# Performance work log

Measured on AMD Instinct MI355X. Metric: run time of the kernel, lower is better.

## Reference

```python
import jax, jax.numpy as jnp
import numpy as np

N, D_IN, D_OUT = 10000, 256, 256


def setup_inputs() -> dict:
    key = jax.random.key(0)
    k1, k2, k3, k4 = jax.random.split(key, 4)
    # xavier_uniform with gain=1.414 (as in the torch module)
    def xavier(k, shape, gain=1.414):
        fan_in, fan_out = shape[0], shape[1]
        bound = gain * np.sqrt(6.0 / (fan_in + fan_out))
        return jax.random.uniform(k, shape, jnp.float32, -bound, bound)
    return {
        "input": jax.random.normal(k1, (N, D_IN), jnp.float32),
        "adj": jax.random.randint(k2, (N, N), 0, 2, jnp.int32),  # binary dense adjacency
        "M": N,
        "W": xavier(k3, (D_IN, D_OUT)),
        "b": jnp.zeros((D_OUT,), jnp.float32),
        "a": xavier(k4, (D_OUT, 1)),
    }


def reference(input, adj, M, W, b, a):
    # h = tanh(X W + b); values used for attention logits
    h = jnp.tanh(input @ W + b)          # [N, F]
    inp = input @ W                      # [N, F] (values to aggregate)
    e = (h @ a)[:, 0]                    # [N] per-node logit
    # original also drops neighbors whose h row sums to exactly 0
    valid = (jnp.sum(h, axis=1) != 0)    # [N]
    mask = (adj[:M] > 0) & valid[None, :]  # [M, N]
    neg = jnp.asarray(-1e30, h.dtype)
    scores = jnp.where(mask, e[None, :], neg)           # [M, N]
    m = jnp.max(scores, axis=1, keepdims=True)
    w = jnp.where(mask, jnp.exp(scores - m), 0.0)       # masked exp
    denom = jnp.sum(w, axis=1, keepdims=True)
    att = w / jnp.maximum(denom, 1e-30)  # rows with no neighbors -> all zeros (matches torch zeros init)
    # dropout is identity in eval mode (training=False)
    return att @ inp                     # [M, F]
```

## Files before the change

### kernel.cpp

```cpp
#include <hip/hip_runtime.h>
#include <hip/hip_bf16.h>
#include <cstdint>
#include <cstddef>

#define NN      10000
#define DD      256
#define KSTEPS  313
#define MB2     79
#define KSPLIT  6

typedef __bf16 bf16x8 __attribute__((ext_vector_type(8)));
typedef float  f32x4  __attribute__((ext_vector_type(4)));

#define XG_OFF   0ull
#define XG_SIZE  (32ull * 10000 * 16)
#define WG_OFF   (XG_OFF + XG_SIZE)
#define WG_SIZE  (32ull * 256 * 16)
#define INP_OFF  (WG_OFF + WG_SIZE)
#define INP_SIZE (10000ull * 256 * 4)
#define E_OFF    (INP_OFF + INP_SIZE)
#define E_SIZE   (10016ull * 4)
#define HS_OFF   (E_OFF + E_SIZE)
#define HS_SIZE  (10016ull * 4)
#define G_OFF    (HS_OFF + HS_SIZE)
#define G_SIZE   (10016ull * 4)
#define YG_OFF   (G_OFF + G_SIZE + 256ull)
#define YG_SIZE  (318ull * 1088 * 16)
#define PN_OFF   (YG_OFF + YG_SIZE)
#define PN_SIZE  ((size_t)KSPLIT * 10000 * 272 * 4)

__device__ __forceinline__ void gl_lds16(const void* g, void* lds) {
    __builtin_amdgcn_global_load_lds(
        (const __attribute__((address_space(1))) unsigned int*)g,
        (__attribute__((address_space(3))) unsigned int*)lds,
        16, 0, 0);
}

__global__ __launch_bounds__(256) void k_build_xg(const float* __restrict__ X,
                                                  bf16x8* __restrict__ XG) {
    int idx = blockIdx.x * 256 + threadIdx.x;
    int row = idx >> 5;
    int q   = idx & 31;
    const float* src = X + row * 256 + q * 8;
    bf16x8 v;
#pragma unroll
    for (int j = 0; j < 8; ++j) v[j] = (__bf16)src[j];
    XG[q * 10000 + row] = v;
}

__global__ __launch_bounds__(256) void k_build_wg(const float* __restrict__ W,
                                                  bf16x8* __restrict__ WG) {
    int e = blockIdx.x * 256 + threadIdx.x;
    int q = e >> 8;
    int n = e & 255;
    bf16x8 v;
#pragma unroll
    for (int j = 0; j < 8; ++j) v[j] = (__bf16)W[(q * 8 + j) * 256 + n];
    WG[e] = v;
}

__global__ __launch_bounds__(256) void k_gemm1(const bf16x8* __restrict__ XG,
                                               const bf16x8* __restrict__ WG,
                                               const float* __restrict__ bvec,
                                               const float* __restrict__ avec,
                                               float* __restrict__ inp,
                                               float* __restrict__ evec,
                                               float* __restrict__ hsumv) {
    __shared__ bf16x8 Ash[320];
    __shared__ bf16x8 Bsh[1024];
    __shared__ float ePart[4][80];
    __shared__ float hPart[4][80];
    int tid = threadIdx.x, wid = tid >> 6, lane = tid & 63;
    int l15 = lane & 15, l4 = lane >> 4;
    int mb = blockIdx.x;

    f32x4 acc[4][5];
#pragma unroll
    for (int c = 0; c < 4; ++c)
#pragma unroll
        for (int rt = 0; rt < 5; ++rt) acc[c][rt] = f32x4{0.f, 0.f, 0.f, 0.f};

    for (int kb = 0; kb < 8; ++kb) {
        for (int rr = wid; rr < 5; rr += 4) {
            int c = rr * 64 + lane;
            int g = c / 80, r = c - g * 80;
            gl_lds16(XG + ((kb * 4 + g) * 10000 + mb * 80 + r), (char*)Ash + rr * 1024);
        }
        for (int rr = wid; rr < 16; rr += 4)
            gl_lds16(WG + kb * 1024 + rr * 64 + lane, (char*)Bsh + rr * 1024);
        __syncthreads();

        bf16x8 af[5];
#pragma unroll
        for (int rt = 0; rt < 5; ++rt) af[rt] = Ash[l4 * 80 + rt * 16 + l15];
#pragma unroll
        for (int c = 0; c < 4; ++c) {
            bf16x8 bf = Bsh[l4 * 256 + (wid * 4 + c) * 16 + l15];
#pragma unroll
            for (int rt = 0; rt < 5; ++rt)
                acc[c][rt] = __builtin_amdgcn_mfma_f32_16x16x32_bf16(af[rt], bf, acc[c][rt], 0, 0, 0);
        }
        __syncthreads();
    }

    float pe[5][4], ph[5][4];
#pragma unroll
    for (int rt = 0; rt < 5; ++rt)
#pragma unroll
        for (int rg = 0; rg < 4; ++rg) { pe[rt][rg] = 0.f; ph[rt][rg] = 0.f; }

#pragma unroll
    for (int c = 0; c < 4; ++c) {
        int col = (wid * 4 + c) * 16 + l15;
        float av = avec[col];
        float bv = bvec[col];
#pragma unroll
        for (int rt = 0; rt < 5; ++rt) {
#pragma unroll
            for (int rg = 0; rg < 4; ++rg) {
                int row = mb * 80 + rt * 16 + l4 * 4 + rg;
                float v = acc[c][rt][rg];
                inp[row * 256 + col] = v;
                float h = tanhf(v + bv);
                pe[rt][rg] += h * av;
                ph[rt][rg] += h;
            }
        }
    }
#pragma unroll
    for (int rt = 0; rt < 5; ++rt) {
#pragma unroll
        for (int rg = 0; rg < 4; ++rg) {
            float se = pe[rt][rg], sh = ph[rt][rg];
#pragma unroll
            for (int m = 1; m < 16; m <<= 1) {
                se += __shfl_xor(se, m);
                sh += __shfl_xor(sh, m);
            }
            if (l15 == 0) {
                int lr = rt * 16 + l4 * 4 + rg;
                ePart[wid][lr] = se;
                hPart[wid][lr] = sh;
            }
        }
    }
    __syncthreads();
    if (tid < 80) {
        float e = ePart[0][tid] + ePart[1][tid] + ePart[2][tid] + ePart[3][tid];
        float h = hPart[0][tid] + hPart[1][tid] + hPart[2][tid] + hPart[3][tid];
        evec[mb * 80 + tid] = e;
        hsumv[mb * 80 + tid] = h;
    }
}

__global__ __launch_bounds__(1024) void k_softmax_g(const float* __restrict__ evec,
                                                    const float* __restrict__ hsumv,
                                                    float* __restrict__ gv) {
    __shared__ float red[1024];
    int tid = threadIdx.x;
    float m = -3.0e38f;
    for (int i = tid; i < NN; i += 1024)
        if (hsumv[i] != 0.0f) m = fmaxf(m, evec[i]);
    red[tid] = m;
    __syncthreads();
    for (int s = 512; s > 0; s >>= 1) {
        if (tid < s) red[tid] = fmaxf(red[tid], red[tid + s]);
        __syncthreads();
    }
    float gmax = red[0];
    if (gmax < -1.0e37f) gmax = 0.0f;
    for (int i = tid; i < 10016; i += 1024) {
        float g = 0.0f;
        if (i < NN && hsumv[i] != 0.0f) g = expf(evec[i] - gmax);
        gv[i] = g;
    }
}

__global__ __launch_bounds__(256) void k_build_yg(const float* __restrict__ inp,
                                                  const float* __restrict__ gv,
                                                  bf16x8* __restrict__ YG) {
    int kb = blockIdx.x;
    for (int c = threadIdx.x; c < 1088; c += 256) {
        int gq = c / 272, n = c - gq * 272;
        int k0 = kb * 32 + gq * 8;
        bf16x8 v;
#pragma unroll
        for (int j = 0; j < 8; ++j) {
            int k = k0 + j;
            float val = 0.0f;
            if (k < NN) {
                float gk = gv[k];
                if (n < 256) val = gk * inp[k * 256 + n];
                else if (n == 256) val = gk;
            }
            v[j] = (__bf16)val;
        }
        YG[kb * 1088 + c] = v;
    }
}

__device__ __forceinline__ bf16x8 cvt_adj(int4 a, int4 b) {
    union { bf16x8 v; unsigned int u[4]; } r;
    r.u[0] = (a.x > 0 ? 0x3F80u : 0u) | (a.y > 0 ? 0x3F800000u : 0u);
    r.u[1] = (a.z > 0 ? 0x3F80u : 0u) | (a.w > 0 ? 0x3F800000u : 0u);
    r.u[2] = (b.x > 0 ? 0x3F80u : 0u) | (b.y > 0 ? 0x3F800000u : 0u);
    r.u[3] = (b.z > 0 ? 0x3F80u : 0u) | (b.w > 0 ? 0x3F800000u : 0u);
    return r.v;
}

__global__ __launch_bounds__(256, 2) void k_attn_gemm(const int* __restrict__ adj,
                                                      const bf16x8* __restrict__ YG,
                                                      float* __restrict__ pnum) {
    __shared__ int    Ash[2][4096];
    __shared__ bf16x8 Bsh[2][1088];
    int tid = threadIdx.x, wid = tid >> 6, lane = tid & 63;
    int l15 = lane & 15, l4 = lane >> 4;

    int orig = blockIdx.x;
    const int nwg = MB2 * KSPLIT, q = nwg >> 3, r = nwg & 7;
    int x = orig & 7, o = orig >> 3;
    int logical = (x < r ? x * (q + 1) : r * (q + 1) + (x - r) * q) + o;
    int kc = logical / MB2, mb = logical % MB2;
    int s0 = (kc * KSTEPS) / KSPLIT, s1 = ((kc + 1) * KSTEPS) / KSPLIT;

    const int* aSrc[4];
    int aLim[4];
#pragma unroll
    for (int i = 0; i < 4; ++i) {
        int c = (wid + i * 4) * 64 + lane;
        int row = c >> 3;
        int p = c & 7;
        int ck4 = (p ^ (row & 7)) * 4;
        int grow = min(mb * 128 + row, NN - 1);
        aSrc[i] = adj + (size_t)grow * 10000 + ck4;
        aLim[i] = 9996 - ck4;
    }

    f32x4 acc[2][17];
#pragma unroll
    for (int t = 0; t < 2; ++t)
#pragma unroll
        for (int ct = 0; ct < 17; ++ct) acc[t][ct] = f32x4{0.f, 0.f, 0.f, 0.f};

    auto stageA = [&](int sTile, int bufIdx) {
        int kk = sTile * 32;
        char* dst = (char*)&Ash[bufIdx][0];
#pragma unroll
        for (int i = 0; i < 4; ++i)
            gl_lds16(aSrc[i] + min(kk, aLim[i]), dst + (wid + i * 4) * 1024);
    };
    auto stageB = [&](int sTile, int bufIdx) {
        const bf16x8* src = YG + (size_t)sTile * 1088;
        char* dst = (char*)&Bsh[bufIdx][0];
#pragma unroll
        for (int i = 0; i < 5; ++i) {
            int rr = wid + i * 4;
            if (rr < 17) gl_lds16(src + rr * 64 + lane, dst + rr * 1024);
        }
    };

    int xr = l15 & 7;
    int p0 = (2 * l4) ^ xr;
    int rowA0 = wid * 32 + l15;

    stageA(s0, 0);
    stageB(s0, 0);
    __syncthreads();

    int buf = 0;
    for (int s = s0; s < s1; ++s) {
        if (s + 1 < s1) {
            stageA(s + 1, buf ^ 1);
            stageB(s + 1, buf ^ 1);
        }
        const int* ab = &Ash[buf][0];
        int4 v00 = *(const int4*)(ab + rowA0 * 32 + p0 * 4);
        int4 v01 = *(const int4*)(ab + rowA0 * 32 + (p0 ^ 1) * 4);
        int4 v10 = *(const int4*)(ab + (rowA0 + 16) * 32 + p0 * 4);
        int4 v11 = *(const int4*)(ab + (rowA0 + 16) * 32 + (p0 ^ 1) * 4);
        bf16x8 fa0 = cvt_adj(v00, v01);
        bf16x8 fa1 = cvt_adj(v10, v11);
#pragma unroll
        for (int ct = 0; ct < 17; ++ct) {
            bf16x8 fb = Bsh[buf][l4 * 272 + ct * 16 + l15];
            acc[0][ct] = __builtin_amdgcn_mfma_f32_16x16x32_bf16(fa0, fb, acc[0][ct], 0, 0, 0);
            acc[1][ct] = __builtin_amdgcn_mfma_f32_16x16x32_bf16(fa1, fb, acc[1][ct], 0, 0, 0);
        }
        __syncthreads();
        buf ^= 1;
    }

    float* base = pnum + (size_t)kc * 10000 * 272;
    int r0 = mb * 128 + wid * 32;
#pragma unroll
    for (int t = 0; t < 2; ++t) {
#pragma unroll
        for (int ct = 0; ct < 17; ++ct) {
            int col = ct * 16 + l15;
#pragma unroll
            for (int rg = 0; rg < 4; ++rg) {
                int row = r0 + t * 16 + l4 * 4 + rg;
                if (row < NN) base[(size_t)row * 272 + col] = acc[t][ct][rg];
            }
        }
    }
}

__global__ __launch_bounds__(256) void k_finalize(const float* __restrict__ pnum,
                                                  float* __restrict__ out) {
    int idx = blockIdx.x * 256 + threadIdx.x;
    int i = idx >> 6, q = idx & 63;
    float4 sv = {0.f, 0.f, 0.f, 0.f};
    float den = 0.f;
#pragma unroll
    for (int kc = 0; kc < KSPLIT; ++kc) {
        const float* row = pnum + ((size_t)kc * 10000 + i) * 272;
        float4 v = ((const float4*)row)[q];
        sv.x += v.x; sv.y += v.y; sv.z += v.z; sv.w += v.w;
        den += row[256];
    }
    float r = 1.0f / fmaxf(den, 1e-30f);
    float4 o;
    o.x = sv.x * r; o.y = sv.y * r; o.z = sv.z * r; o.w = sv.w * r;
    ((float4*)(out + (size_t)i * 256))[q] = o;
}

extern "C" void kernel_launch(void* const* d_in, const int* in_sizes, int n_in,
                              void* d_out, int out_size, void* d_ws, size_t ws_size,
                              hipStream_t stream) {
    const float* X    = (const float*)d_in[0];
    const int*   adj  = (const int*)d_in[1];
    const float* W    = (const float*)d_in[3];
    const float* bvec = (const float*)d_in[4];
    const float* avec = (const float*)d_in[5];
    float* out = (float*)d_out;

    char* ws = (char*)d_ws;
    bf16x8* XG   = (bf16x8*)(ws + XG_OFF);
    bf16x8* WG   = (bf16x8*)(ws + WG_OFF);
    float*  inp  = (float*)(ws + INP_OFF);
    float*  evec = (float*)(ws + E_OFF);
    float*  hsv  = (float*)(ws + HS_OFF);
    float*  gv   = (float*)(ws + G_OFF);
    bf16x8* YG   = (bf16x8*)(ws + YG_OFF);
    float*  pnum = (float*)(ws + PN_OFF);

    k_build_xg<<<1250, 256, 0, stream>>>(X, XG);
    k_build_wg<<<32, 256, 0, stream>>>(W, WG);
    k_gemm1<<<125, 256, 0, stream>>>(XG, WG, bvec, avec, inp, evec, hsv);
    k_softmax_g<<<1, 1024, 0, stream>>>(evec, hsv, gv);
    k_build_yg<<<318, 256, 0, stream>>>(inp, gv, YG);
    k_attn_gemm<<<MB2 * KSPLIT, 256, 0, stream>>>(adj, YG, pnum);
    k_finalize<<<2500, 256, 0, stream>>>(pnum, out);
}
```

Baseline: 191.8 us.

## Fuse prep kernels and replace single-block softmax with atomic global max

Merges the X and W bf16 repacking kernels into one launch, which also zeroes a global max slot. The per-block max of valid logits is now computed inside gemm1 and combined with an order-preserving atomicMax. The exp weights are computed on the fly inside build_yg. This removes two launches, including a serial single-block reduction, at the cost of an atomic per gemm1 block and redundant per-block exp work.

```diff
diff --git a/kernel.cpp b/kernel.cpp
--- a/kernel.cpp
+++ b/kernel.cpp
@@ -22,9 +22,9 @@
 #define E_SIZE   (10016ull * 4)
 #define HS_OFF   (E_OFF + E_SIZE)
 #define HS_SIZE  (10016ull * 4)
-#define G_OFF    (HS_OFF + HS_SIZE)
-#define G_SIZE   (10016ull * 4)
-#define YG_OFF   (G_OFF + G_SIZE + 256ull)
+#define GM_OFF   (HS_OFF + HS_SIZE)
+#define GM_SIZE  (256ull)
+#define YG_OFF   (GM_OFF + GM_SIZE)
 #define YG_SIZE  (318ull * 1088 * 16)
 #define PN_OFF   (YG_OFF + YG_SIZE)
 #define PN_SIZE  ((size_t)KSPLIT * 10000 * 272 * 4)
@@ -36,27 +36,31 @@
         16, 0, 0);
 }
 
-__global__ __launch_bounds__(256) void k_build_xg(const float* __restrict__ X,
-                                                  bf16x8* __restrict__ XG) {
-    int idx = blockIdx.x * 256 + threadIdx.x;
-    int row = idx >> 5;
-    int q   = idx & 31;
-    const float* src = X + row * 256 + q * 8;
-    bf16x8 v;
-#pragma unroll
-    for (int j = 0; j < 8; ++j) v[j] = (__bf16)src[j];
-    XG[q * 10000 + row] = v;
-}
-
-__global__ __launch_bounds__(256) void k_build_wg(const float* __restrict__ W,
-                                                  bf16x8* __restrict__ WG) {
-    int e = blockIdx.x * 256 + threadIdx.x;
-    int q = e >> 8;
-    int n = e & 255;
-    bf16x8 v;
-#pragma unroll
-    for (int j = 0; j < 8; ++j) v[j] = (__bf16)W[(q * 8 + j) * 256 + n];
-    WG[e] = v;
+__global__ __launch_bounds__(256) void k_prep(const float* __restrict__ X,
+                                              bf16x8* __restrict__ XG,
+                                              const float* __restrict__ W,
+                                              bf16x8* __restrict__ WG,
+                                              unsigned int* __restrict__ gmaxU) {
+    int b = blockIdx.x;
+    if (b < 1250) {
+        int idx = b * 256 + threadIdx.x;
+        int row = idx >> 5;
+        int q   = idx & 31;
+        const float* src = X + row * 256 + q * 8;
+        bf16x8 v;
+#pragma unroll
+        for (int j = 0; j < 8; ++j) v[j] = (__bf16)src[j];
+        XG[q * 10000 + row] = v;
+    } else {
+        int e = (b - 1250) * 256 + threadIdx.x;
+        int q = e >> 8;
+        int n = e & 255;
+        bf16x8 v;
+#pragma unroll
+        for (int j = 0; j < 8; ++j) v[j] = (__bf16)W[(q * 8 + j) * 256 + n];
+        WG[e] = v;
+        if (b == 1250 && threadIdx.x == 0) *gmaxU = 0u;
+    }
 }
 
 __global__ __launch_bounds__(256) void k_gemm1(const bf16x8* __restrict__ XG,
@@ -65,7 +69,8 @@
                                                const float* __restrict__ avec,
                                                float* __restrict__ inp,
                                                float* __restrict__ evec,
-                                               float* __restrict__ hsumv) {
+                                               float* __restrict__ hsumv,
+                                               unsigned int* __restrict__ gmaxU) {
     __shared__ bf16x8 Ash[320];
     __shared__ bf16x8 Bsh[1024];
     __shared__ float ePart[4][80];
@@ -150,46 +155,49 @@
         float h = hPart[0][tid] + hPart[1][tid] + hPart[2][tid] + hPart[3][tid];
         evec[mb * 80 + tid] = e;
         hsumv[mb * 80 + tid] = h;
-    }
-}
-
-__global__ __launch_bounds__(1024) void k_softmax_g(const float* __restrict__ evec,
-                                                    const float* __restrict__ hsumv,
-                                                    float* __restrict__ gv) {
-    __shared__ float red[1024];
-    int tid = threadIdx.x;
-    float m = -3.0e38f;
-    for (int i = tid; i < NN; i += 1024)
-        if (hsumv[i] != 0.0f) m = fmaxf(m, evec[i]);
-    red[tid] = m;
+        ePart[0][tid] = (h != 0.0f) ? e : -3.0e38f;
+    }
     __syncthreads();
-    for (int s = 512; s > 0; s >>= 1) {
-        if (tid < s) red[tid] = fmaxf(red[tid], red[tid + s]);
-        __syncthreads();
-    }
-    float gmax = red[0];
-    if (gmax < -1.0e37f) gmax = 0.0f;
-    for (int i = tid; i < 10016; i += 1024) {
+    if (tid == 0) {
+        float m = -3.0e38f;
+        for (int i = 0; i < 80; ++i) m = fmaxf(m, ePart[0][i]);
+        if (m > -2.9e38f) {
+            unsigned int b = __float_as_uint(m);
+            unsigned int u = (b & 0x80000000u) ? ~b : (b | 0x80000000u);
+            atomicMax(gmaxU, u);
+        }
+    }
+}
+
+__global__ __launch_bounds__(256) void k_build_yg(const float* __restrict__ inp,
+                                                  const float* __restrict__ evec,
+                                                  const float* __restrict__ hsumv,
+                                                  const unsigned int* __restrict__ gmaxU,
+                                                  bf16x8* __restrict__ YG) {
+    __shared__ float gsh[32];
+    int kb = blockIdx.x;
+    if (threadIdx.x < 32) {
+        unsigned int gu = *gmaxU;
+        float gmax = 0.0f;
+        if (gu != 0u)
+            gmax = (gu & 0x80000000u) ? __uint_as_float(gu ^ 0x80000000u)
+                                      : __uint_as_float(~gu);
+        int k = kb * 32 + threadIdx.x;
         float g = 0.0f;
-        if (i < NN && hsumv[i] != 0.0f) g = expf(evec[i] - gmax);
-        gv[i] = g;
-    }
-}
-
-__global__ __launch_bounds__(256) void k_build_yg(const float* __restrict__ inp,
-                                                  const float* __restrict__ gv,
-                                                  bf16x8* __restrict__ YG) {
-    int kb = blockIdx.x;
+        if (k < NN && hsumv[k] != 0.0f) g = expf(evec[k] - gmax);
+        gsh[threadIdx.x] = g;
+    }
+    __syncthreads();
     for (int c = threadIdx.x; c < 1088; c += 256) {
         int gq = c / 272, n = c - gq * 272;
-        int k0 = kb * 32 + gq * 8;
+        int j0 = gq * 8;
         bf16x8 v;
 #pragma unroll
         for (int j = 0; j < 8; ++j) {
-            int k = k0 + j;
+            int k = kb * 32 + j0 + j;
             float val = 0.0f;
             if (k < NN) {
-                float gk = gv[k];
+                float gk = gsh[j0 + j];
                 if (n < 256) val = gk * inp[k * 256 + n];
                 else if (n == 256) val = gk;
             }
@@ -341,15 +349,13 @@
     float*  inp  = (float*)(ws + INP_OFF);
     float*  evec = (float*)(ws + E_OFF);
     float*  hsv  = (float*)(ws + HS_OFF);
-    float*  gv   = (float*)(ws + G_OFF);
+    unsigned int* gmaxU = (unsigned int*)(ws + GM_OFF);
     bf16x8* YG   = (bf16x8*)(ws + YG_OFF);
     float*  pnum = (float*)(ws + PN_OFF);
 
-    k_build_xg<<<1250, 256, 0, stream>>>(X, XG);
-    k_build_wg<<<32, 256, 0, stream>>>(W, WG);
-    k_gemm1<<<125, 256, 0, stream>>>(XG, WG, bvec, avec, inp, evec, hsv);
-    k_softmax_g<<<1, 1024, 0, stream>>>(evec, hsv, gv);
-    k_build_yg<<<318, 256, 0, stream>>>(inp, gv, YG);
+    k_prep<<<1282, 256, 0, stream>>>(X, XG, W, WG, gmaxU);
+    k_gemm1<<<125, 256, 0, stream>>>(XG, WG, bvec, avec, inp, evec, hsv, gmaxU);
+    k_build_yg<<<318, 256, 0, stream>>>(inp, evec, hsv, gmaxU, YG);
     k_attn_gemm<<<MB2 * KSPLIT, 256, 0, stream>>>(adj, YG, pnum);
     k_finalize<<<2500, 256, 0, stream>>>(pnum, out);
 }
```

Measured after the change: 174.8 us. 8.9% less time.
